# Kernel tuning notes

Measured on AMD Instinct MI355X. Metric: run time of the kernel, lower is better.

The kernel has to match this reference:

```python
import jax, jax.numpy as jnp
import numpy as np

N = 50000      # nodes
DEG = 16       # avg degree
E = N * DEG    # edges
FIN = 128
FQK = 64
FV = 64
H = 8


def setup_inputs() -> dict:
    key = jax.random.key(0)
    k1, k2, k3, k4 = jax.random.split(key, 4)
    x = jax.random.normal(k1, (N, FIN), dtype=jnp.float32)
    # torch Linear(Fin, 2*Fqk+Fv, bias=False); stored here as [Fin, Ftot] so y = x @ W
    W = jax.random.normal(k2, (FIN, 2 * FQK + FV), dtype=jnp.float32) / np.sqrt(FIN)
    # edges: src sorted and covering all nodes (required by scatter_softmax semantics)
    src = jnp.repeat(jnp.arange(N, dtype=jnp.int32), DEG)
    dest = jax.random.randint(k3, (E,), 0, N, dtype=jnp.int32)
    ei = jnp.stack([src, dest])  # [2, E]
    batch = jnp.sort(jax.random.randint(k4, (N,), 0, 64, dtype=jnp.int32))
    return {"x": x, "W": W, "batch": batch, "ei": ei}


def reference(x, W, batch, ei):
    n = x.shape[0]
    Fh = FQK // H   # per-head qk dim
    Fhv = FV // H   # per-head v dim
    scaling = float(Fh) ** (-0.5)

    qkv = x @ W  # [N, 2*Fqk+Fv]
    q, k, v = jnp.split(qkv, [FQK, 2 * FQK], axis=-1)
    q = (q * scaling).reshape(n, H, Fh)
    k = k.reshape(n, H, Fh)
    v = v.reshape(n, H, Fhv)

    src, dest = ei[0], ei[1]
    qs = q[src]   # [E, H, Fh]
    ks = k[dest]  # [E, H, Fh]
    vs = v[dest]  # [E, H, Fhv]

    aw = jnp.einsum("ehf,ehf->eh", qs, ks)  # per-edge per-head logits

    # segment softmax over src (numerically stable, same math as exp/segsum(exp))
    amax = jax.ops.segment_max(aw, src, num_segments=n)
    ex = jnp.exp(aw - amax[src])
    denom = jax.ops.segment_sum(ex, src, num_segments=n)
    aw = ex / denom[src]  # [E, H]

    out = jax.ops.segment_sum(aw[:, :, None] * vs, src, num_segments=n)  # [N, H, Fhv]
    return out.reshape(n, H * Fhv)
```

## Files before the change

kernel.cpp:

```cpp
#include <hip/hip_runtime.h>
#include <math.h>

#define N_NODES 50000
#define DEG 16
#define E_EDGES (N_NODES * DEG)
#define FIN 128
#define FTOT 192
#define FQK 64
#define FV 64
#define H 8

typedef __attribute__((ext_vector_type(8))) short short8;
typedef __attribute__((ext_vector_type(4))) float float4v;

__device__ inline unsigned short f2bf(float f) {
    unsigned int u = __float_as_uint(f);
    unsigned int r = u + 0x7fffu + ((u >> 16) & 1u);
    return (unsigned short)(r >> 16);
}
__device__ inline float bf2f(unsigned short b) {
    return __uint_as_float(((unsigned int)b) << 16);
}

__global__ void wt_prep(const float* __restrict__ W, unsigned short* __restrict__ Wt) {
    int t = blockIdx.x * 256 + threadIdx.x;
    if (t >= FIN * FTOT) return;
    int k = t / FTOT, n = t % FTOT;
    Wt[n * FIN + k] = f2bf(W[t]);
}

#define LDB 136
#define LDC 194
__global__ __launch_bounds__(256) void gemm_qkv(const float* __restrict__ x,
                                                const unsigned short* __restrict__ Wt,
                                                unsigned short* __restrict__ qkv) {
    __shared__ unsigned short Bt[FTOT * LDB];
    unsigned short* Ct = Bt;
    const int tid = threadIdx.x;

#pragma unroll
    for (int i = 0; i < 12; i++) {
        int c = tid + i * 256;
        int n = c >> 4, off = (c & 15) * 8;
        *(uint4*)(&Bt[n * LDB + off]) = *(const uint4*)(Wt + n * FIN + off);
    }

    const int wave = tid >> 6, lane = tid & 63;
    const int m = lane & 15, q = lane >> 4;
    const int row = blockIdx.x * 64 + wave * 16 + m;
    const int rowc = min(row, N_NODES - 1);

    short8 a[4];
    const float* xr = x + rowc * FIN;
#pragma unroll
    for (int s = 0; s < 4; s++) {
        float4v f0 = *(const float4v*)(xr + s * 32 + q * 8);
        float4v f1 = *(const float4v*)(xr + s * 32 + q * 8 + 4);
        short8 av;
        av[0] = (short)f2bf(f0.x); av[1] = (short)f2bf(f0.y);
        av[2] = (short)f2bf(f0.z); av[3] = (short)f2bf(f0.w);
        av[4] = (short)f2bf(f1.x); av[5] = (short)f2bf(f1.y);
        av[6] = (short)f2bf(f1.z); av[7] = (short)f2bf(f1.w);
        a[s] = av;
    }
    __syncthreads();

    float4v acc[12];
#pragma unroll
    for (int ct = 0; ct < 12; ct++) acc[ct] = (float4v){0.f, 0.f, 0.f, 0.f};
#pragma unroll
    for (int ct = 0; ct < 12; ct++) {
#pragma unroll
        for (int s = 0; s < 4; s++) {
            short8 b = *(const short8*)(&Bt[(ct * 16 + m) * LDB + s * 32 + q * 8]);
            acc[ct] = __builtin_amdgcn_mfma_f32_16x16x32_bf16(a[s], b, acc[ct], 0, 0, 0);
        }
    }
    __syncthreads();

    const int lrow0 = wave * 16 + q * 4;
#pragma unroll
    for (int ct = 0; ct < 12; ct++) {
        const int col = ct * 16 + m;
        int off; float scale;
        if (col < FQK)          { off = col;                      scale = 0.35355339059327373f; }
        else if (col < 2 * FQK) { off = 64 + 2 * (col - 64);      scale = 1.f; }
        else                    { off = 64 + 2 * (col - 128) + 1; scale = 1.f; }
#pragma unroll
        for (int i = 0; i < 4; i++)
            Ct[(lrow0 + i) * LDC + off] = f2bf(acc[ct][i] * scale);
    }
    __syncthreads();

    unsigned int* qg = (unsigned int*)qkv;
    const int base = blockIdx.x * 64;
#pragma unroll
    for (int i = 0; i < 24; i++) {
        int l = tid + i * 256;
        int r = l / 96, dw = l - r * 96;
        if (base + r < N_NODES)
            qg[(size_t)(base + r) * 96 + dw] = *(const unsigned int*)(&Ct[r * LDC + 2 * dw]);
    }
}

__global__ __launch_bounds__(256) void attn(const unsigned short* __restrict__ qkv,
                                            const int* __restrict__ dest,
                                            float* __restrict__ out) {
    const int node = blockIdx.x * 4 + (threadIdx.x >> 6);
    const int lane = threadIdx.x & 63;
    const int half = lane >> 5;
    const int l = lane & 31;
    if (node >= N_NODES) return;

    const unsigned int qw = *(const unsigned int*)(qkv + node * FTOT + 2 * l);
    const float q0 = bf2f((unsigned short)(qw & 0xffffu));
    const float q1 = bf2f((unsigned short)(qw >> 16));
    const int dj = dest[node * DEG + (lane & 15)];

    uint2 kv[8];
#pragma unroll
    for (int t = 0; t < 8; t++) {
        const int d = __shfl(dj, 2 * t + half, 64);
        kv[t] = *(const uint2*)(qkv + d * FTOT + 64 + 4 * l);
    }

    float lg[8];
#pragma unroll
    for (int t = 0; t < 8; t++) {
        const float k0 = bf2f((unsigned short)(kv[t].x & 0xffffu));
        const float k1 = bf2f((unsigned short)(kv[t].y & 0xffffu));
        float p = fmaf(q0, k0, q1 * k1);
        p += __shfl_xor(p, 1, 64);
        p += __shfl_xor(p, 2, 64);
        lg[t] = p;
    }
    float mx = lg[0];
#pragma unroll
    for (int t = 1; t < 8; t++) mx = fmaxf(mx, lg[t]);
    float s = 0.f, o0 = 0.f, o1 = 0.f;
#pragma unroll
    for (int t = 0; t < 8; t++) {
        const float p = __expf(lg[t] - mx);
        s += p;
        o0 = fmaf(p, __uint_as_float(kv[t].x & 0xffff0000u), o0);
        o1 = fmaf(p, __uint_as_float(kv[t].y & 0xffff0000u), o1);
    }
    const float mo = __shfl_xor(mx, 32, 64);
    const float mn = fmaxf(mx, mo);
    const float f = __expf(mx - mn);
    s *= f; o0 *= f; o1 *= f;
    s  += __shfl_xor(s, 32, 64);
    o0 += __shfl_xor(o0, 32, 64);
    o1 += __shfl_xor(o1, 32, 64);
    if (half == 0) {
        float2 r; r.x = o0 / s; r.y = o1 / s;
        *(float2*)(out + node * 64 + 2 * l) = r;
    }
}

extern "C" void kernel_launch(void* const* d_in, const int* in_sizes, int n_in,
                              void* d_out, int out_size, void* d_ws, size_t ws_size,
                              hipStream_t stream) {
    const float* x = (const float*)d_in[0];
    const float* W = (const float*)d_in[1];
    const int* ei = (const int*)d_in[3];
    const int* dest = ei + E_EDGES;
    float* out = (float*)d_out;

    unsigned short* qkv = (unsigned short*)d_ws;
    unsigned short* Wt  = (unsigned short*)((char*)d_ws + 19200000);

    wt_prep<<<(FIN * FTOT + 255) / 256, 256, 0, stream>>>(W, Wt);
    gemm_qkv<<<(N_NODES + 63) / 64, 256, 0, stream>>>(x, Wt, qkv);
    attn<<<(N_NODES + 3) / 4, 256, 0, stream>>>(qkv, dest, out);
}
```

Before: 112.9 us.

## Widen attention gathers to 16-byte loads and pre-pad weight tile layout

The attention kernel now maps 16 lanes per edge, with four edges per wave in parallel, so each lane does one 16-byte K/V gather per edge instead of 8-byte loads. Destination indices are read with one int4 load per quarter-wave rather than being broadcast by shuffles. The softmax uses a single global max across quarters, and the output is written as float4. The weight prep writes a padded LDB layout so the GEMM can copy it into LDS as a flat contiguous block. This costs more cross-lane reduction shuffles at the end, but issues fewer, wider gather instructions.

```diff
diff --git a/kernel.cpp b/kernel.cpp
--- a/kernel.cpp
+++ b/kernel.cpp
@@ -21,16 +21,19 @@
 __device__ inline float bf2f(unsigned short b) {
     return __uint_as_float(((unsigned int)b) << 16);
 }
+__device__ inline float bflo(unsigned int w) { return __uint_as_float(w << 16); }
+__device__ inline float bfhi(unsigned int w) { return __uint_as_float(w & 0xffff0000u); }
+
+#define LDB 136
+#define LDC 194
 
 __global__ void wt_prep(const float* __restrict__ W, unsigned short* __restrict__ Wt) {
     int t = blockIdx.x * 256 + threadIdx.x;
     if (t >= FIN * FTOT) return;
     int k = t / FTOT, n = t % FTOT;
-    Wt[n * FIN + k] = f2bf(W[t]);
+    Wt[n * LDB + k] = f2bf(W[t]);
 }
 
-#define LDB 136
-#define LDC 194
 __global__ __launch_bounds__(256) void gemm_qkv(const float* __restrict__ x,
                                                 const unsigned short* __restrict__ Wt,
                                                 unsigned short* __restrict__ qkv) {
@@ -39,10 +42,10 @@
     const int tid = threadIdx.x;
 
 #pragma unroll
-    for (int i = 0; i < 12; i++) {
+    for (int i = 0; i < 13; i++) {
         int c = tid + i * 256;
-        int n = c >> 4, off = (c & 15) * 8;
-        *(uint4*)(&Bt[n * LDB + off]) = *(const uint4*)(Wt + n * FIN + off);
+        if (c < (FTOT * LDB) / 8)
+            *(uint4*)(&Bt[c * 8]) = *(const uint4*)(Wt + c * 8);
     }
 
     const int wave = tid >> 6, lane = tid & 63;
@@ -108,53 +111,60 @@
                                             float* __restrict__ out) {
     const int node = blockIdx.x * 4 + (threadIdx.x >> 6);
     const int lane = threadIdx.x & 63;
-    const int half = lane >> 5;
-    const int l = lane & 31;
+    const int quarter = lane >> 4;
+    const int l = lane & 15;
     if (node >= N_NODES) return;
 
-    const unsigned int qw = *(const unsigned int*)(qkv + node * FTOT + 2 * l);
-    const float q0 = bf2f((unsigned short)(qw & 0xffffu));
-    const float q1 = bf2f((unsigned short)(qw >> 16));
-    const int dj = dest[node * DEG + (lane & 15)];
+    const uint2 qw = *(const uint2*)(qkv + node * FTOT + 4 * l);
+    const float q0 = bflo(qw.x), q1 = bfhi(qw.x) ;
+    const float q2 = bflo(qw.y), q3 = bfhi(qw.y);
 
-    uint2 kv[8];
-#pragma unroll
-    for (int t = 0; t < 8; t++) {
-        const int d = __shfl(dj, 2 * t + half, 64);
-        kv[t] = *(const uint2*)(qkv + d * FTOT + 64 + 4 * l);
+    const int4 dd = ((const int4*)(dest + (size_t)node * DEG))[quarter];
+
+    uint4 kv[4];
+    {
+        const int d0 = dd.x, d1 = dd.y, d2 = dd.z, d3 = dd.w;
+        kv[0] = *(const uint4*)(qkv + d0 * FTOT + 64 + 8 * l);
+        kv[1] = *(const uint4*)(qkv + d1 * FTOT + 64 + 8 * l);
+        kv[2] = *(const uint4*)(qkv + d2 * FTOT + 64 + 8 * l);
+        kv[3] = *(const uint4*)(qkv + d3 * FTOT + 64 + 8 * l);
     }
 
-    float lg[8];
+    float lg[4];
 #pragma unroll
-    for (int t = 0; t < 8; t++) {
-        const float k0 = bf2f((unsigned short)(kv[t].x & 0xffffu));
-        const float k1 = bf2f((unsigned short)(kv[t].y & 0xffffu));
-        float p = fmaf(q0, k0, q1 * k1);
+    for (int t = 0; t < 4; t++) {
+        float p = q0 * bflo(kv[t].x);
+        p = fmaf(q1, bflo(kv[t].y), p);
+        p = fmaf(q2, bflo(kv[t].z), p);
+        p = fmaf(q3, bflo(kv[t].w), p);
         p += __shfl_xor(p, 1, 64);
-        p += __shfl_xor(p, 2, 64);
         lg[t] = p;
     }
-    float mx = lg[0];
+
+    float m = fmaxf(fmaxf(lg[0], lg[1]), fmaxf(lg[2], lg[3]));
+    m = fmaxf(m, __shfl_xor(m, 16, 64));
+    m = fmaxf(m, __shfl_xor(m, 32, 64));
+
+    float s = 0.f, o0 = 0.f, o1 = 0.f, o2 = 0.f, o3 = 0.f;
 #pragma unroll
-    for (int t = 1; t < 8; t++) mx = fmaxf(mx, lg[t]);
-    float s = 0.f, o0 = 0.f, o1 = 0.f;
-#pragma unroll
-    for (int t = 0; t < 8; t++) {
-        const float p = __expf(lg[t] - mx);
+    for (int t = 0; t < 4; t++) {
+        const float p = __expf(lg[t] - m);
         s += p;
-        o0 = fmaf(p, __uint_as_float(kv[t].x & 0xffff0000u), o0);
-        o1 = fmaf(p, __uint_as_float(kv[t].y & 0xffff0000u), o1);
+        o0 = fmaf(p, bfhi(kv[t].x), o0);
+        o1 = fmaf(p, bfhi(kv[t].y), o1);
+        o2 = fmaf(p, bfhi(kv[t].z), o2);
+        o3 = fmaf(p, bfhi(kv[t].w), o3);
     }
-    const float mo = __shfl_xor(mx, 32, 64);
-    const float mn = fmaxf(mx, mo);
-    const float f = __expf(mx - mn);
-    s *= f; o0 *= f; o1 *= f;
-    s  += __shfl_xor(s, 32, 64);
-    o0 += __shfl_xor(o0, 32, 64);
-    o1 += __shfl_xor(o1, 32, 64);
-    if (half == 0) {
-        float2 r; r.x = o0 / s; r.y = o1 / s;
-        *(float2*)(out + node * 64 + 2 * l) = r;
+    s  += __shfl_xor(s, 16, 64);  s  += __shfl_xor(s, 32, 64);
+    o0 += __shfl_xor(o0, 16, 64); o0 += __shfl_xor(o0, 32, 64);
+    o1 += __shfl_xor(o1, 16, 64); o1 += __shfl_xor(o1, 32, 64);
+    o2 += __shfl_xor(o2, 16, 64); o2 += __shfl_xor(o2, 32, 64);
+    o3 += __shfl_xor(o3, 16, 64); o3 += __shfl_xor(o3, 32, 64);
+
+    if (quarter == 0) {
+        const float inv = 1.0f / s;
+        float4 r; r.x = o0 * inv; r.y = o1 * inv; r.z = o2 * inv; r.w = o3 * inv;
+        *(float4*)(out + node * 64 + 4 * l) = r;
     }
 }
 
```

Result: no change. 114.1 us (+1.1%).
